# Kernel tuning notes

Hardware: AMD Instinct MI355X
Metric: run time of the kernel (lower is better)

Reference implementation:

```python
import jax, jax.numpy as jnp
import numpy as np
from jax import lax

L = 8
PATCH = 3
DIRS = [(0, 1), (1, 0), (1, 1), (1, -1)]


def _pair_indices():
    coords = np.arange(PATCH * PATCH)
    rr, cc = coords // PATCH, coords % PATCH
    i1s, i2s = [], []
    for dr, dc in DIRS:
        m = (rr + dr >= 0) & (rr + dr < PATCH) & (cc + dc >= 0) & (cc + dc < PATCH)
        i1s.append(coords[m])
        i2s.append((rr[m] + dr) * PATCH + (cc[m] + dc))
    return np.concatenate(i1s), np.concatenate(i2s)

_I1, _I2 = _pair_indices()


def conv_bn_silu(x, w, s, b, pad):
    # Conv2d(bias=False) + eval-mode BatchNorm folded into (s, b) + SiLU
    y = lax.conv_general_dilated(x, w, (1, 1), [(pad, pad), (pad, pad)],
                                 dimension_numbers=("NCHW", "OIHW", "NCHW"))
    y = y * s[None, :, None, None] + b[None, :, None, None]
    return jax.nn.silu(y)


def glcm_feats(x):
    B, C, H, W = x.shape
    pad = PATCH // 2
    xp = jnp.pad(x, ((0, 0), (0, 0), (pad, pad), (pad, pad)), mode="edge")
    # unfold: (B, C, 9, H, W)
    patches = jnp.stack([xp[:, :, i:i + H, j:j + W]
                         for i in range(PATCH) for j in range(PATCH)], axis=2)
    q = jnp.clip((patches * (L - 1)).astype(jnp.int32), 0, L - 1)
    q = q.reshape(B * C, PATCH * PATCH, H * W)
    # co-occurrence pair indices for all 4 directions, concatenated: (BC, K, HW)
    idx = q[:, _I1, :] * L + q[:, _I2, :]
    idx = idx.transpose(0, 2, 1)  # (BC, HW, K)
    # per-pixel local histogram over L*L bins (scatter-add)
    hist = jax.vmap(jax.vmap(
        lambda v: jnp.zeros((L * L,), x.dtype).at[v].add(1.0)))(idx)
    hist = hist / len(DIRS)  # reduce_mode='average'
    s = jnp.maximum(hist.sum(-1, keepdims=True), 1e-6)
    p = hist / s  # (BC, HW, L*L)
    li = jnp.arange(L, dtype=x.dtype)
    diff = li[:, None] - li[None, :]
    diff_sq = (diff ** 2).reshape(-1)
    abs_d = jnp.abs(diff).reshape(-1)
    contrast = (p * diff_sq).sum(-1)
    energy = (p * p).sum(-1)
    entropy = -(p * jnp.log(p + 1e-6)).sum(-1)
    homog = (p / (1.0 + abs_d)).sum(-1)
    f = jnp.stack([contrast, energy, entropy, homog], axis=-1)  # (BC, HW, 4)
    f = f.reshape(B, C, H * W, 4).mean(axis=1)  # average over channels
    return f.transpose(0, 2, 1).reshape(B, 4, H, W)


def setup_inputs() -> dict:
    key = jax.random.key(0)
    B, C, H, W = 4, 64, 80, 80
    c_, cb, c2 = 32, 16, 64
    ks = iter(jax.random.split(key, 20))
    x = jax.random.uniform(next(ks), (B, C, H, W), jnp.float32)

    def conv_p(cin, cout, ksz):
        w = jax.random.normal(next(ks), (cout, cin, ksz, ksz), jnp.float32) / np.sqrt(cin * ksz * ksz)
        s = jax.random.uniform(next(ks), (cout,), jnp.float32, 0.5, 1.5)
        b = jax.random.normal(next(ks), (cout,), jnp.float32) * 0.1
        return w, s, b

    cv1_w, cv1_s, cv1_b = conv_p(C + 4, c_, 1)
    cv2_w, cv2_s, cv2_b = conv_p(C + 4, c_, 1)
    m1_w, m1_s, m1_b = conv_p(c_, cb, 1)
    m2_w, m2_s, m2_b = conv_p(cb, c_, 3)
    cv3_w, cv3_s, cv3_b = conv_p(2 * c_, c2, 1)
    return dict(x=x, cv1_w=cv1_w, cv1_s=cv1_s, cv1_b=cv1_b,
                cv2_w=cv2_w, cv2_s=cv2_s, cv2_b=cv2_b,
                m1_w=m1_w, m1_s=m1_s, m1_b=m1_b,
                m2_w=m2_w, m2_s=m2_s, m2_b=m2_b,
                cv3_w=cv3_w, cv3_s=cv3_s, cv3_b=cv3_b)


def reference(x, cv1_w, cv1_s, cv1_b, cv2_w, cv2_s, cv2_b,
              m1_w, m1_s, m1_b, m2_w, m2_s, m2_b,
              cv3_w, cv3_s, cv3_b):
    g = glcm_feats(x)
    xc = jnp.concatenate([x, g], axis=1)  # (B, C+4, H, W)
    a = conv_bn_silu(xc, cv1_w, cv1_s, cv1_b, 0)
    y = conv_bn_silu(a, m1_w, m1_s, m1_b, 0)
    y = conv_bn_silu(y, m2_w, m2_s, m2_b, 1)
    a = a + y  # Bottleneck shortcut (c1 == c2)
    b = conv_bn_silu(xc, cv2_w, cv2_s, cv2_b, 0)
    return conv_bn_silu(jnp.concatenate([a, b], axis=1), cv3_w, cv3_s, cv3_b, 0)
```

## Files before the change

### kernel.cpp

```cpp
#include <hip/hip_runtime.h>
#include <math.h>

constexpr int B = 4, C = 64, H = 80, W = 80;
constexpr int HW = H * W;
constexpr int NPIX = B * HW;

typedef unsigned u32;

static __device__ __forceinline__ float silu(float v) {
    float e = __expf(-v);
    return v * __builtin_amdgcn_rcpf(1.0f + e);
}

static __device__ __forceinline__ u32 pks(u32 a, u32 b){u32 d; asm("v_pk_sub_u16 %0,%1,%2":"=v"(d):"v"(a),"v"(b)); return d;}
static __device__ __forceinline__ u32 pka(u32 a, u32 b){u32 d; asm("v_pk_add_u16 %0,%1,%2":"=v"(d):"v"(a),"v"(b)); return d;}
static __device__ __forceinline__ u32 pkm(u32 a, u32 b){u32 d; asm("v_pk_mul_lo_u16 %0,%1,%2":"=v"(d):"v"(a),"v"(b)); return d;}
static __device__ __forceinline__ u32 pkmin(u32 a, u32 b){u32 d; asm("v_pk_min_u16 %0,%1,%2":"=v"(d):"v"(a),"v"(b)); return d;}
static __device__ __forceinline__ u32 pkmaxi(u32 a, u32 b){u32 d; asm("v_pk_max_i16 %0,%1,%2":"=v"(d):"v"(a),"v"(b)); return d;}
static __device__ __forceinline__ float cb0(u32 a){float f; asm("v_cvt_f32_ubyte0 %0,%1":"=v"(f):"v"(a)); return f;}
static __device__ __forceinline__ float cb2(u32 a){float f; asm("v_cvt_f32_ubyte2 %0,%1":"=v"(f):"v"(a)); return f;}

static __device__ __forceinline__ void ce(u32 &x, u32 &y) {
    u32 mn, mx;
    asm("v_pk_min_u16 %0, %2, %3\n\t"
        "v_pk_max_u16 %1, %2, %3"
        : "=&v"(mn), "=v"(mx) : "v"(x), "v"(y));
    x = mn; y = mx;
}

__global__ __launch_bounds__(256) void glcm_kernel(const float* __restrict__ x,
                                                   float* __restrict__ g) {
    const int t = threadIdx.x;
    const int pxl = t & 7;
    const int grp = t >> 3;
    const int pix = blockIdx.x * 8 + pxl;
    const int b = pix / HW;
    const int hw = pix - b * HW;
    const int h = hw / W;
    const int w = hw - h * W;
    const int hm = h > 0 ? h - 1 : 0;
    const int hp = h < H - 1 ? h + 1 : H - 1;
    const int wm = w > 0 ? w - 1 : 0;
    const int wp = w < W - 1 ? w + 1 : W - 1;
    const int o[9] = {hm * W + wm, hm * W + w, hm * W + wp,
                      h  * W + wm, h  * W + w, h  * W + wp,
                      hp * W + wm, hp * W + w, hp * W + wp};
    const float* c0 = x + (size_t)(b * C + grp * 2) * HW;
    const float* c1 = c0 + HW;

    u32 qpk[9];
    #pragma unroll
    for (int k = 0; k < 9; ++k) {
        int a0 = (int)(c0[o[k]] * 7.0f);
        int a1 = (int)(c1[o[k]] * 7.0f);
        a0 = a0 < 0 ? 0 : (a0 > 7 ? 7 : a0);
        a1 = a1 < 0 ? 0 : (a1 > 7 ? 7 : a1);
        qpk[k] = (u32)a0 | ((u32)a1 << 16);
    }

    static constexpr int PA[20] = {0,1,3,4,6,7, 0,1,2,3,4,5, 0,1,3,4, 1,2,4,5};
    static constexpr int PB[20] = {1,2,4,5,7,8, 3,4,5,6,7,8, 4,5,7,8, 3,4,6,7};

    const u32 ONEpk = 0x00010001u, EIGHTpk = 0x00080008u;
    u32 cs = 0;
    float hsum = 0.f;
    u32 key[20];
    #pragma unroll
    for (int a = 0; a < 20; ++a) {
        const u32 qa = qpk[PA[a]], qb = qpk[PB[a]];
        const u32 d = pks(qa, qb);
        cs = pka(cs, pkm(d, d));
        const u32 ad = pkmaxi(d, pks(0u, d));
        const u32 h1 = pka(ad, ONEpk);
        hsum += __builtin_amdgcn_rcpf(cb0(h1)) + __builtin_amdgcn_rcpf(cb2(h1));
        key[a] = pka(pkm(qa, EIGHTpk), qb);
    }

    #pragma unroll
    for (int p = 1; p < 32; p <<= 1) {
        #pragma unroll
        for (int k = p; k >= 1; k >>= 1) {
            const int jm = k % p;
            #pragma unroll
            for (int lo = 0; lo < 20; ++lo) {
                const int hi = lo + k;
                if (hi < 20 && lo >= jm && ((lo - jm) % (2 * k)) < k &&
                    (lo / (2 * p)) == (hi / (2 * p))) {
                    ce(key[lo], key[hi]);
                }
            }
        }
    }

    u32 eq[20];
    #pragma unroll
    for (int a = 1; a < 20; ++a)
        eq[a] = pks(ONEpk, pkmin(pks(key[a], key[a - 1]), ONEpk));

    u32 pc = 0, ps = 0, pv[20];
    pv[0] = 0;
    #pragma unroll
    for (int a = 1; a < 20; ++a) {
        pc = pkm(pka(pc, ONEpk), eq[a]);
        pv[a] = pc;
        ps = pka(ps, pc);
    }
    float pr0, pr1;
    {
        const u32 m = pka(pv[19], ONEpk);
        pr0 = cb0(m); pr1 = cb2(m);
    }
    u32 rc = 0;
    #pragma unroll
    for (int a = 18; a >= 0; --a) {
        rc = pkm(pka(rc, ONEpk), eq[a + 1]);
        const u32 m = pka(pka(pv[a], rc), ONEpk);
        pr0 *= cb0(m); pr1 *= cb2(m);
    }

    const int csum = (int)(cs & 0xFFFFu) + (int)(cs >> 16);
    const int psum = (int)(ps & 0xFFFFu) + (int)(ps >> 16);
    const float lsum = __logf(pr0) + __logf(pr1);

    float fc = (float)csum * (1.f / 20.f);
    float fe = ((float)psum * 2.f + 40.f) * (1.f / 400.f);
    float fn = -(lsum + 40.f * -2.9957322736f ) * (1.f / 20.f);
    float fh = hsum * (1.f / 20.f);

    #pragma unroll
    for (int m = 8; m < 64; m <<= 1) {
        fc += __shfl_xor(fc, m);
        fe += __shfl_xor(fe, m);
        fn += __shfl_xor(fn, m);
        fh += __shfl_xor(fh, m);
    }
    __shared__ float red[4][8][4];
    const int wv = t >> 6;
    if ((t & 63) < 8) {
        red[wv][pxl][0] = fc; red[wv][pxl][1] = fe;
        red[wv][pxl][2] = fn; red[wv][pxl][3] = fh;
    }
    __syncthreads();
    if (t < 32) {
        const int p2 = t >> 2, f = t & 3;
        float s = red[0][p2][f] + red[1][p2][f] + red[2][p2][f] + red[3][p2][f];
        s *= (1.f / 64.f);
        const int pix2 = blockIdx.x * 8 + p2;
        const int b2 = pix2 / HW;
        const int hw2 = pix2 - b2 * HW;
        g[((size_t)(b2 * 4 + f)) * HW + hw2] = s;
    }
}

__global__ __launch_bounds__(512) void stage1_kernel(
    const float* __restrict__ x, const float* __restrict__ g,
    const float* __restrict__ w1, const float* __restrict__ s1, const float* __restrict__ b1,
    const float* __restrict__ w2, const float* __restrict__ s2, const float* __restrict__ b2,
    const float* __restrict__ wm1, const float* __restrict__ sm1, const float* __restrict__ bm1,
    float* __restrict__ a, float* __restrict__ bbuf, float* __restrict__ y16) {
    __shared__ float xg[68][64];
    __shared__ float aT[32][64];
    const int t = threadIdx.x;
    const int p0 = blockIdx.x * 64;
    const int bi = p0 / HW;
    const int hw0 = p0 - bi * HW;

    const float* xb = x + (size_t)(bi * C) * HW + hw0;
    const float* gb = g + (size_t)(bi * 4) * HW + hw0;
    #pragma unroll
    for (int rnd = 0; rnd < 9; ++rnd) {
        const int e = rnd * 512 + t;
        if (e < 68 * 64) {
            const int ic = e >> 6, px = e & 63;
            xg[ic][px] = (ic < 64) ? xb[(size_t)ic * HW + px]
                                   : gb[(size_t)(ic - 64) * HW + px];
        }
    }
    __syncthreads();

    const int lane = t & 63;
    const int wv = __builtin_amdgcn_readfirstlane(t >> 6);
    const int oc0 = wv * 4;
    const int hw = hw0 + lane;

    float acc1[4] = {0.f, 0.f, 0.f, 0.f};
    float acc2[4] = {0.f, 0.f, 0.f, 0.f};
    #pragma unroll 4
    for (int ic = 0; ic < 68; ++ic) {
        const float v = xg[ic][lane];
        #pragma unroll
        for (int j = 0; j < 4; ++j) {
            acc1[j] += v * w1[(oc0 + j) * 68 + ic];
            acc2[j] += v * w2[(oc0 + j) * 68 + ic];
        }
    }
    #pragma unroll
    for (int j = 0; j < 4; ++j) {
        const int oc = oc0 + j;
        const float v1 = silu(acc1[j] * s1[oc] + b1[oc]);
        a[((size_t)(bi * 32 + oc)) * HW + hw] = v1;
        aT[oc][lane] = v1;
        bbuf[((size_t)(bi * 32 + oc)) * HW + hw] = silu(acc2[j] * s2[oc] + b2[oc]);
    }
    __syncthreads();
    const int om0 = wv * 2;
    float am0 = 0.f, am1 = 0.f;
    #pragma unroll 4
    for (int ic = 0; ic < 32; ++ic) {
        const float v = aT[ic][lane];
        am0 += v * wm1[om0 * 32 + ic];
        am1 += v * wm1[(om0 + 1) * 32 + ic];
    }
    y16[((size_t)(bi * 16 + om0)) * HW + hw]     = silu(am0 * sm1[om0] + bm1[om0]);
    y16[((size_t)(bi * 16 + om0 + 1)) * HW + hw] = silu(am1 * sm1[om0 + 1] + bm1[om0 + 1]);
}

__global__ __launch_bounds__(512) void m2cv3_kernel(
    const float* __restrict__ y16, const float* __restrict__ a,
    const float* __restrict__ bbuf,
    const float* __restrict__ wm2, const float* __restrict__ sm2, const float* __restrict__ bm2,
    const float* __restrict__ wc, const float* __restrict__ sc, const float* __restrict__ bc,
    float* __restrict__ out) {
    __shared__ float ys[16][4][82];
    __shared__ float a2[32][64];
    __shared__ float bs[32][64];
    const int t = threadIdx.x;
    const int p0 = blockIdx.x * 64;
    const int bi = p0 / HW;
    const int hw0 = p0 - bi * HW;
    const int h0 = hw0 / W;

    const float* yb = y16 + (size_t)(bi * 16) * HW;
    for (int e = t; e < 16 * 4 * 82; e += 512) {
        const int ch = e / 328;
        const int rem = e - ch * 328;
        const int row = rem / 82;
        const int col = rem - row * 82;
        const int r = h0 - 1 + row;
        const int c = col - 1;
        float v = 0.f;
        if ((unsigned)r < (unsigned)H && (unsigned)c < (unsigned)W)
            v = yb[(size_t)ch * HW + r * W + c];
        ys[ch][row][col] = v;
    }
    for (int e = t; e < 32 * 64; e += 512) {
        const int ic = e >> 6, px = e & 63;
        bs[ic][px] = bbuf[((size_t)(bi * 32 + ic)) * HW + hw0 + px];
    }
    __syncthreads();

    const int lane = t & 63;
    const int wv = __builtin_amdgcn_readfirstlane(t >> 6);
    const int hw = hw0 + lane;
    const int h = hw / W;
    const int w = hw - h * W;
    const int lr = h - h0;
    const int oc0 = wv * 4;

    float acc[4] = {0.f, 0.f, 0.f, 0.f};
    #pragma unroll 2
    for (int ic = 0; ic < 16; ++ic) {
        #pragma unroll
        for (int ky = 0; ky < 3; ++ky) {
            #pragma unroll
            for (int kx = 0; kx < 3; ++kx) {
                const float v = ys[ic][lr + ky][w + kx];
                const int tap = ic * 9 + ky * 3 + kx;
                #pragma unroll
                for (int j = 0; j < 4; ++j)
                    acc[j] += v * wm2[(oc0 + j) * 144 + tap];
            }
        }
    }
    #pragma unroll
    for (int j = 0; j < 4; ++j) {
        const int oc = oc0 + j;
        a2[oc][lane] = a[((size_t)(bi * 32 + oc)) * HW + hw]
                     + silu(acc[j] * sm2[oc] + bm2[oc]);
    }
    __syncthreads();
    const int oc3 = wv * 8;
    float c_[8] = {0.f, 0.f, 0.f, 0.f, 0.f, 0.f, 0.f, 0.f};
    #pragma unroll 4
    for (int ic = 0; ic < 32; ++ic) {
        const float av = a2[ic][lane];
        const float bv = bs[ic][lane];
        #pragma unroll
        for (int j = 0; j < 8; ++j) {
            c_[j] += av * wc[(oc3 + j) * 64 + ic];
            c_[j] += bv * wc[(oc3 + j) * 64 + 32 + ic];
        }
    }
    #pragma unroll
    for (int j = 0; j < 8; ++j) {
        const int oc = oc3 + j;
        out[((size_t)(bi * 64 + oc)) * HW + hw] = silu(c_[j] * sc[oc] + bc[oc]);
    }
}

extern "C" void kernel_launch(void* const* d_in, const int* in_sizes, int n_in,
                              void* d_out, int out_size, void* d_ws, size_t ws_size,
                              hipStream_t stream) {
    const float* x    = (const float*)d_in[0];
    const float* cv1w = (const float*)d_in[1];
    const float* cv1s = (const float*)d_in[2];
    const float* cv1b = (const float*)d_in[3];
    const float* cv2w = (const float*)d_in[4];
    const float* cv2s = (const float*)d_in[5];
    const float* cv2b = (const float*)d_in[6];
    const float* m1w  = (const float*)d_in[7];
    const float* m1s  = (const float*)d_in[8];
    const float* m1b  = (const float*)d_in[9];
    const float* m2w  = (const float*)d_in[10];
    const float* m2s  = (const float*)d_in[11];
    const float* m2b  = (const float*)d_in[12];
    const float* cv3w = (const float*)d_in[13];
    const float* cv3s = (const float*)d_in[14];
    const float* cv3b = (const float*)d_in[15];

    float* ws   = (float*)d_ws;
    float* g    = ws;
    float* a    = ws + 102400;
    float* bbuf = ws + 921600;
    float* y16  = ws + 1740800;

    glcm_kernel<<<NPIX / 8, 256, 0, stream>>>(x, g);
    stage1_kernel<<<NPIX / 64, 512, 0, stream>>>(x, g, cv1w, cv1s, cv1b,
                                                 cv2w, cv2s, cv2b,
                                                 m1w, m1s, m1b, a, bbuf, y16);
    m2cv3_kernel<<<NPIX / 64, 512, 0, stream>>>(y16, a, bbuf, m2w, m2s, m2b,
                                                cv3w, cv3s, cv3b, (float*)d_out);
}
```

Measured before the change: 61.91 us.

## Fuse GLCM feature kernel with first 1x1 conv stage

Merges the GLCM feature kernel and the cv1/cv2/m1 pointwise conv stage into one kernel working on 8 pixels per block. The centre pixel values and GLCM features stay in shared memory instead of going through global memory. This removes a launch and the g buffer round trip. In exchange, every small block reloads and transposes all the conv weights into LDS, and output stores are only 8 pixels wide per channel.

```diff
diff --git a/kernel.cpp b/kernel.cpp
--- a/kernel.cpp
+++ b/kernel.cpp
@@ -28,9 +28,32 @@
     x = mn; y = mx;
 }
 
-__global__ __launch_bounds__(256) void glcm_kernel(const float* __restrict__ x,
-                                                   float* __restrict__ g) {
+__global__ __launch_bounds__(256) void glcm_stage1_kernel(
+    const float* __restrict__ x,
+    const float* __restrict__ w1, const float* __restrict__ s1, const float* __restrict__ b1,
+    const float* __restrict__ w2, const float* __restrict__ s2, const float* __restrict__ b2,
+    const float* __restrict__ wm1, const float* __restrict__ sm1, const float* __restrict__ bm1,
+    float* __restrict__ a, float* __restrict__ bbuf, float* __restrict__ y16) {
+    __shared__ float ws1T[68 * 33];
+    __shared__ float ws2T[68 * 33];
+    __shared__ float wsm1T[32 * 17];
+    __shared__ float xs[68][8];
+    __shared__ float aT[32][8];
+    __shared__ float red[4][8][4];
+
     const int t = threadIdx.x;
+
+    {
+        const int oc = t >> 3, i0 = t & 7;
+        for (int ic = i0; ic < 68; ic += 8) {
+            ws1T[ic * 33 + oc] = w1[oc * 68 + ic];
+            ws2T[ic * 33 + oc] = w2[oc * 68 + ic];
+        }
+        if (oc < 16)
+            for (int ic = i0; ic < 32; ic += 8)
+                wsm1T[ic * 17 + oc] = wm1[oc * 32 + ic];
+    }
+
     const int pxl = t & 7;
     const int grp = t >> 3;
     const int pix = blockIdx.x * 8 + pxl;
@@ -51,8 +74,14 @@
     u32 qpk[9];
     #pragma unroll
     for (int k = 0; k < 9; ++k) {
-        int a0 = (int)(c0[o[k]] * 7.0f);
-        int a1 = (int)(c1[o[k]] * 7.0f);
+        const float v0 = c0[o[k]];
+        const float v1 = c1[o[k]];
+        if (k == 4) {
+            xs[grp * 2][pxl] = v0;
+            xs[grp * 2 + 1][pxl] = v1;
+        }
+        int a0 = (int)(v0 * 7.0f);
+        int a1 = (int)(v1 * 7.0f);
         a0 = a0 < 0 ? 0 : (a0 > 7 ? 7 : a0);
         a1 = a1 < 0 ? 0 : (a1 > 7 ? 7 : a1);
         qpk[k] = (u32)a0 | ((u32)a1 << 16);
@@ -66,14 +95,14 @@
     float hsum = 0.f;
     u32 key[20];
     #pragma unroll
-    for (int a = 0; a < 20; ++a) {
-        const u32 qa = qpk[PA[a]], qb = qpk[PB[a]];
+    for (int ai = 0; ai < 20; ++ai) {
+        const u32 qa = qpk[PA[ai]], qb = qpk[PB[ai]];
         const u32 d = pks(qa, qb);
         cs = pka(cs, pkm(d, d));
         const u32 ad = pkmaxi(d, pks(0u, d));
         const u32 h1 = pka(ad, ONEpk);
         hsum += __builtin_amdgcn_rcpf(cb0(h1)) + __builtin_amdgcn_rcpf(cb2(h1));
-        key[a] = pka(pkm(qa, EIGHTpk), qb);
+        key[ai] = pka(pkm(qa, EIGHTpk), qb);
     }
 
     #pragma unroll
@@ -94,15 +123,15 @@
 
     u32 eq[20];
     #pragma unroll
-    for (int a = 1; a < 20; ++a)
-        eq[a] = pks(ONEpk, pkmin(pks(key[a], key[a - 1]), ONEpk));
+    for (int ai = 1; ai < 20; ++ai)
+        eq[ai] = pks(ONEpk, pkmin(pks(key[ai], key[ai - 1]), ONEpk));
 
     u32 pc = 0, ps = 0, pv[20];
     pv[0] = 0;
     #pragma unroll
-    for (int a = 1; a < 20; ++a) {
-        pc = pkm(pka(pc, ONEpk), eq[a]);
-        pv[a] = pc;
+    for (int ai = 1; ai < 20; ++ai) {
+        pc = pkm(pka(pc, ONEpk), eq[ai]);
+        pv[ai] = pc;
         ps = pka(ps, pc);
     }
     float pr0, pr1;
@@ -112,9 +141,9 @@
     }
     u32 rc = 0;
     #pragma unroll
-    for (int a = 18; a >= 0; --a) {
-        rc = pkm(pka(rc, ONEpk), eq[a + 1]);
-        const u32 m = pka(pka(pv[a], rc), ONEpk);
+    for (int ai = 18; ai >= 0; --ai) {
+        rc = pkm(pka(rc, ONEpk), eq[ai + 1]);
+        const u32 m = pka(pka(pv[ai], rc), ONEpk);
         pr0 *= cb0(m); pr1 *= cb2(m);
     }
 
@@ -124,7 +153,7 @@
 
     float fc = (float)csum * (1.f / 20.f);
     float fe = ((float)psum * 2.f + 40.f) * (1.f / 400.f);
-    float fn = -(lsum + 40.f * -2.9957322736f ) * (1.f / 20.f);
+    float fn = -(lsum + 40.f * -2.9957322736f) * (1.f / 20.f);
     float fh = hsum * (1.f / 20.f);
 
     #pragma unroll
@@ -134,7 +163,6 @@
         fn += __shfl_xor(fn, m);
         fh += __shfl_xor(fh, m);
     }
-    __shared__ float red[4][8][4];
     const int wv = t >> 6;
     if ((t & 63) < 8) {
         red[wv][pxl][0] = fc; red[wv][pxl][1] = fe;
@@ -144,75 +172,42 @@
     if (t < 32) {
         const int p2 = t >> 2, f = t & 3;
         float s = red[0][p2][f] + red[1][p2][f] + red[2][p2][f] + red[3][p2][f];
-        s *= (1.f / 64.f);
-        const int pix2 = blockIdx.x * 8 + p2;
-        const int b2 = pix2 / HW;
-        const int hw2 = pix2 - b2 * HW;
-        g[((size_t)(b2 * 4 + f)) * HW + hw2] = s;
-    }
-}
-
-__global__ __launch_bounds__(512) void stage1_kernel(
-    const float* __restrict__ x, const float* __restrict__ g,
-    const float* __restrict__ w1, const float* __restrict__ s1, const float* __restrict__ b1,
-    const float* __restrict__ w2, const float* __restrict__ s2, const float* __restrict__ b2,
-    const float* __restrict__ wm1, const float* __restrict__ sm1, const float* __restrict__ bm1,
-    float* __restrict__ a, float* __restrict__ bbuf, float* __restrict__ y16) {
-    __shared__ float xg[68][64];
-    __shared__ float aT[32][64];
-    const int t = threadIdx.x;
-    const int p0 = blockIdx.x * 64;
-    const int bi = p0 / HW;
-    const int hw0 = p0 - bi * HW;
-
-    const float* xb = x + (size_t)(bi * C) * HW + hw0;
-    const float* gb = g + (size_t)(bi * 4) * HW + hw0;
-    #pragma unroll
-    for (int rnd = 0; rnd < 9; ++rnd) {
-        const int e = rnd * 512 + t;
-        if (e < 68 * 64) {
-            const int ic = e >> 6, px = e & 63;
-            xg[ic][px] = (ic < 64) ? xb[(size_t)ic * HW + px]
-                                   : gb[(size_t)(ic - 64) * HW + px];
-        }
-    }
-    __syncthreads();
-
-    const int lane = t & 63;
-    const int wv = __builtin_amdgcn_readfirstlane(t >> 6);
-    const int oc0 = wv * 4;
-    const int hw = hw0 + lane;
-
-    float acc1[4] = {0.f, 0.f, 0.f, 0.f};
-    float acc2[4] = {0.f, 0.f, 0.f, 0.f};
-    #pragma unroll 4
-    for (int ic = 0; ic < 68; ++ic) {
-        const float v = xg[ic][lane];
-        #pragma unroll
-        for (int j = 0; j < 4; ++j) {
-            acc1[j] += v * w1[(oc0 + j) * 68 + ic];
-            acc2[j] += v * w2[(oc0 + j) * 68 + ic];
-        }
-    }
-    #pragma unroll
-    for (int j = 0; j < 4; ++j) {
-        const int oc = oc0 + j;
-        const float v1 = silu(acc1[j] * s1[oc] + b1[oc]);
-        a[((size_t)(bi * 32 + oc)) * HW + hw] = v1;
-        aT[oc][lane] = v1;
-        bbuf[((size_t)(bi * 32 + oc)) * HW + hw] = silu(acc2[j] * s2[oc] + b2[oc]);
-    }
-    __syncthreads();
-    const int om0 = wv * 2;
-    float am0 = 0.f, am1 = 0.f;
-    #pragma unroll 4
-    for (int ic = 0; ic < 32; ++ic) {
-        const float v = aT[ic][lane];
-        am0 += v * wm1[om0 * 32 + ic];
-        am1 += v * wm1[(om0 + 1) * 32 + ic];
-    }
-    y16[((size_t)(bi * 16 + om0)) * HW + hw]     = silu(am0 * sm1[om0] + bm1[om0]);
-    y16[((size_t)(bi * 16 + om0 + 1)) * HW + hw] = silu(am1 * sm1[om0 + 1] + bm1[om0 + 1]);
+        xs[64 + f][p2] = s * (1.f / 64.f);
+    }
+    __syncthreads();
+
+    {
+        const int px = t & 7;
+        const int oc = t >> 3;
+        float acc1 = 0.f, acc2 = 0.f;
+        #pragma unroll 4
+        for (int ic = 0; ic < 68; ++ic) {
+            const float v = xs[ic][px];
+            acc1 += v * ws1T[ic * 33 + oc];
+            acc2 += v * ws2T[ic * 33 + oc];
+        }
+        const int pix2 = blockIdx.x * 8 + px;
+        const int bb = pix2 / HW;
+        const int hw2 = pix2 - bb * HW;
+        const float v1 = silu(acc1 * s1[oc] + b1[oc]);
+        a[((size_t)(bb * 32 + oc)) * HW + hw2] = v1;
+        aT[oc][px] = v1;
+        bbuf[((size_t)(bb * 32 + oc)) * HW + hw2] = silu(acc2 * s2[oc] + b2[oc]);
+    }
+    __syncthreads();
+
+    if (t < 128) {
+        const int px = t & 7;
+        const int oc = t >> 3;
+        float acc = 0.f;
+        #pragma unroll 4
+        for (int ic = 0; ic < 32; ++ic)
+            acc += aT[ic][px] * wsm1T[ic * 17 + oc];
+        const int pix2 = blockIdx.x * 8 + px;
+        const int bb = pix2 / HW;
+        const int hw2 = pix2 - bb * HW;
+        y16[((size_t)(bb * 16 + oc)) * HW + hw2] = silu(acc * sm1[oc] + bm1[oc]);
+    }
 }
 
 __global__ __launch_bounds__(512) void m2cv3_kernel(
@@ -319,15 +314,12 @@
     const float* cv3b = (const float*)d_in[15];
 
     float* ws   = (float*)d_ws;
-    float* g    = ws;
-    float* a    = ws + 102400;
-    float* bbuf = ws + 921600;
-    float* y16  = ws + 1740800;
-
-    glcm_kernel<<<NPIX / 8, 256, 0, stream>>>(x, g);
-    stage1_kernel<<<NPIX / 64, 512, 0, stream>>>(x, g, cv1w, cv1s, cv1b,
-                                                 cv2w, cv2s, cv2b,
-                                                 m1w, m1s, m1b, a, bbuf, y16);
+    float* a    = ws;
+    float* bbuf = ws + 819200;
+    float* y16  = ws + 1638400;
+
+    glcm_stage1_kernel<<<NPIX / 8, 256, 0, stream>>>(
+        x, cv1w, cv1s, cv1b, cv2w, cv2s, cv2b, m1w, m1s, m1b, a, bbuf, y16);
     m2cv3_kernel<<<NPIX / 64, 512, 0, stream>>>(y16, a, bbuf, m2w, m2s, m2b,
                                                 cv3w, cv3s, cv3b, (float*)d_out);
 }
```

Measured after the change: 61.35 us. About the same (-0.9%).
